# Kernel tuning notes

Hardware: AMD Instinct MI355X
Metric: run time of the kernel (lower is better)

The kernel has to match this reference:

```python
import jax, jax.numpy as jnp
import numpy as np

B, T, I, H, C = 64, 2048, 128, 256, 64


def setup_inputs() -> dict:
    key = jax.random.key(0)
    ks = jax.random.split(key, 12)
    s_ih = 1.0 / np.sqrt(H)
    inp = {
        "x": jax.random.normal(ks[0], (B, T, I), dtype=jnp.float32),
        # layer 0 GRU params (PyTorch layout: W_ih [3H, I], W_hh [3H, H])
        "W_ih0": jax.random.uniform(ks[1], (3 * H, I), minval=-s_ih, maxval=s_ih, dtype=jnp.float32),
        "W_hh0": jax.random.uniform(ks[2], (3 * H, H), minval=-s_ih, maxval=s_ih, dtype=jnp.float32),
        "b_ih0": jax.random.uniform(ks[3], (3 * H,), minval=-s_ih, maxval=s_ih, dtype=jnp.float32),
        "b_hh0": jax.random.uniform(ks[4], (3 * H,), minval=-s_ih, maxval=s_ih, dtype=jnp.float32),
        # layer 1 GRU params (input is H)
        "W_ih1": jax.random.uniform(ks[5], (3 * H, H), minval=-s_ih, maxval=s_ih, dtype=jnp.float32),
        "W_hh1": jax.random.uniform(ks[6], (3 * H, H), minval=-s_ih, maxval=s_ih, dtype=jnp.float32),
        "b_ih1": jax.random.uniform(ks[7], (3 * H,), minval=-s_ih, maxval=s_ih, dtype=jnp.float32),
        "b_hh1": jax.random.uniform(ks[8], (3 * H,), minval=-s_ih, maxval=s_ih, dtype=jnp.float32),
        # classifier head
        "fc_w": jax.random.uniform(ks[9], (C, H), minval=-s_ih, maxval=s_ih, dtype=jnp.float32),
        "fc_b": jax.random.uniform(ks[10], (C,), minval=-s_ih, maxval=s_ih, dtype=jnp.float32),
    }
    return inp


def _gru_layer(inp, W_ih, W_hh, b_ih, b_hh):
    # inp: [B, T, D_in] -> out: [B, T, H]; PyTorch GRU cell math.
    h_dim = W_hh.shape[1]
    # Precompute input-side gate pre-activations for the whole sequence (one big GEMM).
    gates_x = jnp.einsum("btd,gd->btg", inp, W_ih) + b_ih  # [B, T, 3H]

    def step(h, gx):
        gh = h @ W_hh.T + b_hh  # [B, 3H]
        xr, xz, xn = jnp.split(gx, 3, axis=-1)
        hr, hz, hn = jnp.split(gh, 3, axis=-1)
        r = jax.nn.sigmoid(xr + hr)
        z = jax.nn.sigmoid(xz + hz)
        n = jnp.tanh(xn + r * hn)
        h_new = (1.0 - z) * n + z * h
        return h_new, h_new

    h0 = jnp.zeros((inp.shape[0], h_dim), dtype=inp.dtype)
    _, out_tbh = jax.lax.scan(step, h0, jnp.swapaxes(gates_x, 0, 1))  # [T, B, H]
    return jnp.swapaxes(out_tbh, 0, 1)  # [B, T, H]


def reference(x, W_ih0, W_hh0, b_ih0, b_hh0, W_ih1, W_hh1, b_ih1, b_hh1, fc_w, fc_b):
    h = _gru_layer(x, W_ih0, W_hh0, b_ih0, b_hh0)
    h = _gru_layer(h, W_ih1, W_hh1, b_ih1, b_hh1)
    return h @ fc_w.T + fc_b  # [B, T, C]
```

## Files before the change

### kernel.cpp

```cpp
#include <hip/hip_runtime.h>

typedef _Float16 half2_t __attribute__((ext_vector_type(2)));
typedef _Float16 half8_t __attribute__((ext_vector_type(8)));
typedef float floatx4 __attribute__((ext_vector_type(4)));
typedef unsigned int u32;

#define BB 64
#define TT 2048
#define II 128
#define HH 256
#define CC 64
#define G3 (3*HH)
#define MTOT (BB*TT)

static __device__ __forceinline__ float dot2f(half2_t a, half2_t b, float c) {
#if __has_builtin(__builtin_amdgcn_fdot2)
    return __builtin_amdgcn_fdot2(a, b, c, false);
#else
    return c + (float)a[0]*(float)b[0] + (float)a[1]*(float)b[1];
#endif
}

static __device__ __forceinline__ half2_t bch2(u32 x) {
    return __builtin_bit_cast(half2_t, x);
}

static __device__ __forceinline__ float fast_rcp(float x) {
    return __builtin_amdgcn_rcpf(x);
}

static __device__ __forceinline__ float pair_sum(float x) {
    int i = __builtin_bit_cast(int, x);
    int a = __builtin_amdgcn_mov_dpp(i, 0xB1, 0xF, 0xF, true);
    return x + __builtin_bit_cast(float, a);
}
static __device__ __forceinline__ float dpp_xor2(float x) {
    int i = __builtin_bit_cast(int, x);
    int a = __builtin_amdgcn_mov_dpp(i, 0x4E, 0xF, 0xF, true);
    return __builtin_bit_cast(float, a);
}

template<typename AT, typename CT>
__global__ __launch_bounds__(256, 2)
void gemm_mfma(const AT* __restrict__ A, const float* __restrict__ W,
               const float* __restrict__ bias, CT* __restrict__ Cout,
               int M, int N, int K)
{
    __shared__ alignas(16) u32 As32[128 * 32];
    __shared__ alignas(16) u32 Bs32[64 * 32];

    const int tid  = threadIdx.x;
    const int lane = tid & 63;
    const int wave = tid >> 6;
    const int wm   = wave >> 1;
    const int wn   = wave & 1;
    const int m0   = blockIdx.y * 128;
    const int n0   = blockIdx.x * 64;
    const int lr   = lane & 15;
    const int lg   = lane >> 4;

    floatx4 acc[4][2] = {};

    for (int kc = 0; kc < K; kc += 64) {
        #pragma unroll
        for (int it = 0; it < 4; ++it) {
            const int s    = it * 256 + tid;
            const int row  = s >> 3;
            const int slot = s & 7;
            const AT* src  = A + (size_t)(m0 + row) * K + kc + slot * 8;
            half8_t v;
            if constexpr (sizeof(AT) == 2) {
                v = *reinterpret_cast<const half8_t*>(src);
            } else {
                const float4* s4 = reinterpret_cast<const float4*>(src);
                float4 lo = s4[0], hi = s4[1];
                v[0] = (_Float16)lo.x; v[1] = (_Float16)lo.y;
                v[2] = (_Float16)lo.z; v[3] = (_Float16)lo.w;
                v[4] = (_Float16)hi.x; v[5] = (_Float16)hi.y;
                v[6] = (_Float16)hi.z; v[7] = (_Float16)hi.w;
            }
            const int sw = slot ^ (row & 7);
            *reinterpret_cast<half8_t*>(&As32[row * 32 + sw * 4]) = v;
        }
        #pragma unroll
        for (int it = 0; it < 2; ++it) {
            const int s    = it * 256 + tid;
            const int row  = s >> 3;
            const int slot = s & 7;
            const float* src = W + (size_t)(n0 + row) * K + kc + slot * 8;
            const float4* s4 = reinterpret_cast<const float4*>(src);
            float4 lo = s4[0], hi = s4[1];
            half8_t v;
            v[0] = (_Float16)lo.x; v[1] = (_Float16)lo.y;
            v[2] = (_Float16)lo.z; v[3] = (_Float16)lo.w;
            v[4] = (_Float16)hi.x; v[5] = (_Float16)hi.y;
            v[6] = (_Float16)hi.z; v[7] = (_Float16)hi.w;
            const int sw = slot ^ (row & 7);
            *reinterpret_cast<half8_t*>(&Bs32[row * 32 + sw * 4]) = v;
        }
        __syncthreads();

        #pragma unroll
        for (int ks = 0; ks < 2; ++ks) {
            half8_t af[4], bf[2];
            #pragma unroll
            for (int fm = 0; fm < 4; ++fm) {
                const int row  = wm * 64 + fm * 16 + lr;
                const int slot = ks * 4 + lg;
                const int sw   = slot ^ (row & 7);
                af[fm] = *reinterpret_cast<const half8_t*>(&As32[row * 32 + sw * 4]);
            }
            #pragma unroll
            for (int fn = 0; fn < 2; ++fn) {
                const int row  = wn * 32 + fn * 16 + lr;
                const int slot = ks * 4 + lg;
                const int sw   = slot ^ (row & 7);
                bf[fn] = *reinterpret_cast<const half8_t*>(&Bs32[row * 32 + sw * 4]);
            }
            #pragma unroll
            for (int fm = 0; fm < 4; ++fm)
                #pragma unroll
                for (int fn = 0; fn < 2; ++fn)
                    acc[fm][fn] = __builtin_amdgcn_mfma_f32_16x16x32_f16(
                        af[fm], bf[fn], acc[fm][fn], 0, 0, 0);
        }
        __syncthreads();
    }

    #pragma unroll
    for (int fn = 0; fn < 2; ++fn) {
        const int n = n0 + wn * 32 + fn * 16 + lr;
        const float bv = bias[n];
        #pragma unroll
        for (int fm = 0; fm < 4; ++fm) {
            #pragma unroll
            for (int r = 0; r < 4; ++r) {
                const int m = m0 + wm * 64 + fm * 16 + lg * 4 + r;
                Cout[(size_t)m * N + n] = (CT)(acc[fm][fn][r] + bv);
            }
        }
    }
}

__global__ __attribute__((amdgpu_flat_work_group_size(512, 512),
                          amdgpu_waves_per_eu(2, 2)))
void gru_scan(const _Float16* __restrict__ gx,
              const float* __restrict__ Whh,
              const float* __restrict__ bhh,
              _Float16* __restrict__ hout)
{
    const int b  = blockIdx.x;
    const int t  = threadIdx.x;
    const int j  = t >> 1;
    const int kh = t & 1;

    __shared__ alignas(16) u32 WzL[512 * 68];
    __shared__ alignas(16) u32 HsU[2][136];

    half2_t w0[64], w2[64];
    {
        const float2* q0 = reinterpret_cast<const float2*>(Whh + (size_t)j * HH + kh * 128);
        const float2* q2 = q0 + 256 * HH;
        #pragma unroll
        for (int i = 0; i < 64; ++i) {
            const float2 a = q0[i], d = q2[i];
            w0[i] = half2_t{(_Float16)a.x, (_Float16)a.y};
            w2[i] = half2_t{(_Float16)d.x, (_Float16)d.y};
        }
    }
    {
        const float2* q1 = reinterpret_cast<const float2*>(Whh + (size_t)(256 + j) * HH + kh * 128);
        u32* wz = WzL + t * 68;
        #pragma unroll
        for (int i = 0; i < 64; ++i) {
            const float2 c = q1[i];
            const half2_t hp{(_Float16)c.x, (_Float16)c.y};
            wz[i] = __builtin_bit_cast(u32, hp);
        }
    }
    const float bh_r = bhh[j], bh_z = bhh[HH + j], bh_n = bhh[2*HH + j];

    if (t < 272) reinterpret_cast<u32*>(HsU)[t] = 0u;
    float hprev = 0.f;

    const _Float16* gp = gx + (size_t)b * TT * G3 + j;
    u32* opw = (u32*)(hout + (size_t)b * TT * HH);

    _Float16 pxr = gp[0], pxz = gp[HH], pxn = gp[2*HH];
    __syncthreads();

    for (int step = 0; step < TT; ++step) {
        const _Float16 nxr = gp[G3];
        const _Float16 nxz = gp[G3 + HH];
        const _Float16 nxn = gp[G3 + 2*HH];

        const uint4* hb  = reinterpret_cast<const uint4*>(HsU[step & 1] + kh * 68);
        const uint4* wzv = reinterpret_cast<const uint4*>(WzL + t * 68);
        float ar = 0.f, az = 0.f, an = 0.f;
        #pragma unroll
        for (int c = 0; c < 16; ++c) {
            const uint4 hv = hb[c];
            const uint4 wv = wzv[c];
            const half2_t ha = bch2(hv.x), hc = bch2(hv.y);
            const half2_t hd = bch2(hv.z), he = bch2(hv.w);
            ar = dot2f(ha, w0[4*c+0], ar); az = dot2f(ha, bch2(wv.x), az); an = dot2f(ha, w2[4*c+0], an);
            ar = dot2f(hc, w0[4*c+1], ar); az = dot2f(hc, bch2(wv.y), az); an = dot2f(hc, w2[4*c+1], an);
            ar = dot2f(hd, w0[4*c+2], ar); az = dot2f(hd, bch2(wv.z), az); an = dot2f(hd, w2[4*c+2], an);
            ar = dot2f(he, w0[4*c+3], ar); az = dot2f(he, bch2(wv.w), az); an = dot2f(he, w2[4*c+3], an);
        }
        ar = pair_sum(ar);
        az = pair_sum(az);
        an = pair_sum(an);

        const float r = fast_rcp(1.f + __expf(-((float)pxr + ar + bh_r)));
        const float z = fast_rcp(1.f + __expf(-((float)pxz + az + bh_z)));
        const float e = __expf(2.f * ((float)pxn + r * (an + bh_n)));
        const float n = 1.f - 2.f * fast_rcp(e + 1.f);
        const float hnew = (1.f - z) * n + z * hprev;
        hprev = hnew;

        const float hoth = dpp_xor2(hnew);
        if ((t & 3) == 0) {
            const half2_t hp{(_Float16)hnew, (_Float16)hoth};
            const u32 pu = __builtin_bit_cast(u32, hp);
            const int m = t >> 2;
            HsU[(step + 1) & 1][(m >> 6) * 68 + (m & 63)] = pu;
            opw[m] = pu;
        }
        __syncthreads();

        gp += G3; opw += HH/2;
        pxr = nxr; pxz = nxz; pxn = nxn;
    }
}

extern "C" void kernel_launch(void* const* d_in, const int* in_sizes, int n_in,
                              void* d_out, int out_size, void* d_ws, size_t ws_size,
                              hipStream_t stream) {
    const float* x    = (const float*)d_in[0];
    const float* Wih0 = (const float*)d_in[1];
    const float* Whh0 = (const float*)d_in[2];
    const float* bih0 = (const float*)d_in[3];
    const float* bhh0 = (const float*)d_in[4];
    const float* Wih1 = (const float*)d_in[5];
    const float* Whh1 = (const float*)d_in[6];
    const float* bih1 = (const float*)d_in[7];
    const float* bhh1 = (const float*)d_in[8];
    const float* fcw  = (const float*)d_in[9];
    const float* fcb  = (const float*)d_in[10];
    float* out = (float*)d_out;

    _Float16* gxbuf = (_Float16*)d_ws;
    _Float16* hbuf  = (_Float16*)((char*)d_ws + (size_t)MTOT * G3 * sizeof(_Float16));

    const dim3 blk(256);
    gemm_mfma<float, _Float16><<<dim3(G3/64, MTOT/128), blk, 0, stream>>>(
        x, Wih0, bih0, gxbuf, MTOT, G3, II);
    gru_scan<<<dim3(BB), dim3(512), 0, stream>>>(gxbuf, Whh0, bhh0, hbuf);
    gemm_mfma<_Float16, _Float16><<<dim3(G3/64, MTOT/128), blk, 0, stream>>>(
        hbuf, Wih1, bih1, gxbuf, MTOT, G3, HH);
    gru_scan<<<dim3(BB), dim3(512), 0, stream>>>(gxbuf, Whh1, bhh1, hbuf);
    gemm_mfma<_Float16, float><<<dim3(CC/64, MTOT/128), blk, 0, stream>>>(
        hbuf, fcw, fcb, out, MTOT, CC, HH);
}
```

Before: 4.840 ms.

## Compute GRU n-gate recurrent matvec with MFMA and keep z weights in registers

The n-gate part of the recurrent h·W_hh product moves from per-thread fp16 dot2 accumulation to 16x16x32 fp16 MFMA. The h vector is broadcast across all 16 A rows, so most of each MFMA's output is redundant. Each result is reduced through a small shared-memory buffer and read back within the same wave. Freeing those registers lets the z-gate weights, previously streamed from LDS every step, live in registers, which removes most per-step LDS traffic. The cost is wasted MFMA work, higher VGPR pressure, and a cross-lane LDS handoff with no explicit barrier.

```diff
diff --git a/kernel.cpp b/kernel.cpp
--- a/kernel.cpp
+++ b/kernel.cpp
@@ -149,37 +149,47 @@
               const float* __restrict__ bhh,
               _Float16* __restrict__ hout)
 {
-    const int b  = blockIdx.x;
-    const int t  = threadIdx.x;
-    const int j  = t >> 1;
-    const int kh = t & 1;
-
-    __shared__ alignas(16) u32 WzL[512 * 68];
-    __shared__ alignas(16) u32 HsU[2][136];
-
-    half2_t w0[64], w2[64];
+    const int b    = blockIdx.x;
+    const int t    = threadIdx.x;
+    const int wv   = t >> 6;
+    const int lane = t & 63;
+    const int lr   = lane & 15;
+    const int lg   = lane >> 4;
+    const int j    = t >> 1;
+    const int kh   = t & 1;
+
+    half2_t wr[64], wz[64];
     {
         const float2* q0 = reinterpret_cast<const float2*>(Whh + (size_t)j * HH + kh * 128);
-        const float2* q2 = q0 + 256 * HH;
+        const float2* q1 = q0 + 128 * HH;
         #pragma unroll
         for (int i = 0; i < 64; ++i) {
-            const float2 a = q0[i], d = q2[i];
-            w0[i] = half2_t{(_Float16)a.x, (_Float16)a.y};
-            w2[i] = half2_t{(_Float16)d.x, (_Float16)d.y};
-        }
-    }
-    {
-        const float2* q1 = reinterpret_cast<const float2*>(Whh + (size_t)(256 + j) * HH + kh * 128);
-        u32* wz = WzL + t * 68;
-        #pragma unroll
-        for (int i = 0; i < 64; ++i) {
-            const float2 c = q1[i];
-            const half2_t hp{(_Float16)c.x, (_Float16)c.y};
-            wz[i] = __builtin_bit_cast(u32, hp);
+            const float2 a = q0[i], c = q1[i];
+            wr[i] = half2_t{(_Float16)a.x, (_Float16)a.y};
+            wz[i] = half2_t{(_Float16)c.x, (_Float16)c.y};
+        }
+    }
+    half8_t wn0[8], wn1[8];
+    #pragma unroll
+    for (int p = 0; p < 2; ++p) {
+        const int row = 512 + wv * 32 + p * 16 + lr;
+        #pragma unroll
+        for (int kf = 0; kf < 8; ++kf) {
+            const float* src = Whh + (size_t)row * HH + kf * 32 + lg * 8;
+            const float4 lo = reinterpret_cast<const float4*>(src)[0];
+            const float4 hi = reinterpret_cast<const float4*>(src)[1];
+            half8_t v;
+            v[0] = (_Float16)lo.x; v[1] = (_Float16)lo.y;
+            v[2] = (_Float16)lo.z; v[3] = (_Float16)lo.w;
+            v[4] = (_Float16)hi.x; v[5] = (_Float16)hi.y;
+            v[6] = (_Float16)hi.z; v[7] = (_Float16)hi.w;
+            if (p == 0) wn0[kf] = v; else wn1[kf] = v;
         }
     }
     const float bh_r = bhh[j], bh_z = bhh[HH + j], bh_n = bhh[2*HH + j];
 
+    __shared__ alignas(16) u32 HsU[2][136];
+    __shared__ float NRed[8][32];
     if (t < 272) reinterpret_cast<u32*>(HsU)[t] = 0u;
     float hprev = 0.f;
 
@@ -194,23 +204,37 @@
         const _Float16 nxz = gp[G3 + HH];
         const _Float16 nxn = gp[G3 + 2*HH];
 
-        const uint4* hb  = reinterpret_cast<const uint4*>(HsU[step & 1] + kh * 68);
-        const uint4* wzv = reinterpret_cast<const uint4*>(WzL + t * 68);
-        float ar = 0.f, az = 0.f, an = 0.f;
+        const u32* hbase = HsU[step & 1];
+
+        floatx4 an0 = {}, an1 = {};
+        #pragma unroll
+        for (int kf = 0; kf < 8; ++kf) {
+            const int off = (kf < 4 ? kf * 16 : 68 + (kf - 4) * 16) + lg * 4;
+            const half8_t a = *reinterpret_cast<const half8_t*>(&hbase[off]);
+            an0 = __builtin_amdgcn_mfma_f32_16x16x32_f16(a, wn0[kf], an0, 0, 0, 0);
+            an1 = __builtin_amdgcn_mfma_f32_16x16x32_f16(a, wn1[kf], an1, 0, 0, 0);
+        }
+
+        const uint4* hb = reinterpret_cast<const uint4*>(hbase + kh * 68);
+        float ar = 0.f, az = 0.f;
         #pragma unroll
         for (int c = 0; c < 16; ++c) {
             const uint4 hv = hb[c];
-            const uint4 wv = wzv[c];
             const half2_t ha = bch2(hv.x), hc = bch2(hv.y);
             const half2_t hd = bch2(hv.z), he = bch2(hv.w);
-            ar = dot2f(ha, w0[4*c+0], ar); az = dot2f(ha, bch2(wv.x), az); an = dot2f(ha, w2[4*c+0], an);
-            ar = dot2f(hc, w0[4*c+1], ar); az = dot2f(hc, bch2(wv.y), az); an = dot2f(hc, w2[4*c+1], an);
-            ar = dot2f(hd, w0[4*c+2], ar); az = dot2f(hd, bch2(wv.z), az); an = dot2f(hd, w2[4*c+2], an);
-            ar = dot2f(he, w0[4*c+3], ar); az = dot2f(he, bch2(wv.w), az); an = dot2f(he, w2[4*c+3], an);
+            ar = dot2f(ha, wr[4*c+0], ar); az = dot2f(ha, wz[4*c+0], az);
+            ar = dot2f(hc, wr[4*c+1], ar); az = dot2f(hc, wz[4*c+1], az);
+            ar = dot2f(hd, wr[4*c+2], ar); az = dot2f(hd, wz[4*c+2], az);
+            ar = dot2f(he, wr[4*c+3], ar); az = dot2f(he, wz[4*c+3], az);
         }
         ar = pair_sum(ar);
         az = pair_sum(az);
-        an = pair_sum(an);
+
+        if (lane < 16) {
+            NRed[wv][lr]      = an0[0];
+            NRed[wv][16 + lr] = an1[0];
+        }
+        const float an = NRed[wv][(t >> 1) & 31];
 
         const float r = fast_rcp(1.f + __expf(-((float)pxr + ar + bh_r)));
         const float z = fast_rcp(1.f + __expf(-((float)pxz + az + bh_z)));
```

After: 5.744 ms. +18.7%, slower.
